# Kernel optimization log

Measured on AMD Instinct MI355X. Metric: run time of the kernel, lower is better.

The kernel has to match this reference:

```python
import jax, jax.numpy as jnp
import numpy as np

N_EMBD = 1024
HEAD_SIZE = 128


def setup_inputs() -> dict:
    key = jax.random.key(0)
    k_x, k_w, k_cov, k_b = jax.random.split(key, 4)
    x = jax.random.normal(k_x, (16384, 2, N_EMBD), dtype=jnp.float32)
    # values_proj: nn.Linear(n_embd, head_size, bias=False) -> weight [head_size, n_embd]
    W = jax.random.normal(k_w, (HEAD_SIZE, N_EMBD), dtype=jnp.float32) * (N_EMBD ** -0.5)
    cov = jax.random.normal(k_cov, (HEAD_SIZE, HEAD_SIZE), dtype=jnp.float32) * (HEAD_SIZE ** -0.5)
    bias = jax.random.normal(k_b, (HEAD_SIZE,), dtype=jnp.float32)
    return {"x": x, "W": W, "cov": cov, "bias": bias}


def reference(x, W, cov, bias):
    # x: [B, 2, E]; W: [H, E]; cov: [H, H]; bias: [H]
    values = jnp.einsum('be,he->bh', x[:, 0, :], W)  # [B, H]
    mask = jnp.einsum('be,he->bh', x[:, 1, :], W)    # [B, H]
    # diag_embed(mask) @ cov == mask[:, :, None] * cov  -> [B, H, H]
    coeffs = jax.nn.softmax(mask[:, :, None] * cov[None, :, :], axis=-1)
    # values.unsqueeze(1) @ coeffs + bias, then [:, 0, :]
    out = jnp.einsum('bh,bhk->bk', values, coeffs) + bias
    return out
```

## Files before the change

kernel.cpp:

```cpp
#include <hip/hip_runtime.h>
#include <hip/hip_bf16.h>

#define LOG2E 1.4426950408889634f

typedef __attribute__((ext_vector_type(8))) short frag_ab;
typedef __attribute__((ext_vector_type(4))) float frag_cd;

__device__ inline short f2bf(float f) {
    union { float f; unsigned u; } v; v.f = f;
    unsigned r = v.u + 0x7fffu + ((v.u >> 16) & 1u);
    return (short)(r >> 16);
}

__global__ __launch_bounds__(256) void prep_kernel(const float* __restrict__ W,
                                                   const float* __restrict__ cov,
                                                   short* __restrict__ wbf,
                                                   float* __restrict__ rmm) {
    if (blockIdx.x < 64) {
        int g = blockIdx.x * 256 + threadIdx.x;
        int h = g >> 7;
        int k0 = (g & 127) << 3;
        const float* src = W + h * 1024 + k0;
        float4 w0 = *(const float4*)src;
        float4 w1 = *(const float4*)(src + 4);
        frag_ab af;
        af[0] = f2bf(w0.x); af[1] = f2bf(w0.y); af[2] = f2bf(w0.z); af[3] = f2bf(w0.w);
        af[4] = f2bf(w1.x); af[5] = f2bf(w1.y); af[6] = f2bf(w1.z); af[7] = f2bf(w1.w);
        int c = k0 >> 6, s = (k0 >> 5) & 1, kg = (k0 >> 3) & 3;
        int nt = h >> 4, m = h & 15, lane = kg * 16 + m;
        int dst = (((c * 8 + nt) * 2 + s) * 64 + lane) * 8;
        *(frag_ab*)(wbf + dst) = af;
    } else {
        int h = blockIdx.x - 64;
        int lane = threadIdx.x;
        if (lane < 64) {
            float c1 = cov[h * 128 + lane];
            float c2 = cov[h * 128 + 64 + lane];
            float mx = fmaxf(c1, c2), mn = fminf(c1, c2);
            for (int o = 1; o < 64; o <<= 1) {
                mx = fmaxf(mx, __shfl_xor(mx, o, 64));
                mn = fminf(mn, __shfl_xor(mn, o, 64));
            }
            if (lane == 0) { rmm[h] = LOG2E * mx; rmm[128 + h] = LOG2E * mn; }
        }
    }
}

__global__ __launch_bounds__(256) void proj_kernel(const float* __restrict__ x,
                                                   const short* __restrict__ wbf,
                                                   float* __restrict__ vm) {
    const int tid = threadIdx.x;
    const int lane = tid & 63;
    const int wave = tid >> 6;
    const int m = lane & 15, kg = lane >> 4;
    const long rowbase = ((long)blockIdx.x * 4 + wave) * 16;
    const float* xrow = x + (rowbase + m) * 1024 + kg * 8;
    const char* wb = (const char*)wbf + lane * 16;

    frag_cd acc[8];
#pragma unroll
    for (int nt = 0; nt < 8; ++nt) acc[nt] = (frag_cd){0.f, 0.f, 0.f, 0.f};

    float4 a0 = *(const float4*)(xrow);
    float4 a1 = *(const float4*)(xrow + 4);
    float4 a2 = *(const float4*)(xrow + 32);
    float4 a3 = *(const float4*)(xrow + 36);

    for (int c = 0; c < 16; ++c) {
        frag_ab bfr[16];
        const char* bc = wb + c * 16384;
#pragma unroll
        for (int f = 0; f < 16; ++f)
            bfr[f] = *(const frag_ab*)(bc + f * 1024);

        float4 n0, n1, n2, n3;
        if (c < 15) {
            const float* xn = xrow + (c + 1) * 64;
            n0 = *(const float4*)(xn);
            n1 = *(const float4*)(xn + 4);
            n2 = *(const float4*)(xn + 32);
            n3 = *(const float4*)(xn + 36);
        }

        frag_ab af0, af1;
        af0[0] = f2bf(a0.x); af0[1] = f2bf(a0.y); af0[2] = f2bf(a0.z); af0[3] = f2bf(a0.w);
        af0[4] = f2bf(a1.x); af0[5] = f2bf(a1.y); af0[6] = f2bf(a1.z); af0[7] = f2bf(a1.w);
        af1[0] = f2bf(a2.x); af1[1] = f2bf(a2.y); af1[2] = f2bf(a2.z); af1[3] = f2bf(a2.w);
        af1[4] = f2bf(a3.x); af1[5] = f2bf(a3.y); af1[6] = f2bf(a3.z); af1[7] = f2bf(a3.w);

#pragma unroll
        for (int nt = 0; nt < 8; ++nt) {
            acc[nt] = __builtin_amdgcn_mfma_f32_16x16x32_bf16(af0, bfr[nt * 2 + 0], acc[nt], 0, 0, 0);
            acc[nt] = __builtin_amdgcn_mfma_f32_16x16x32_bf16(af1, bfr[nt * 2 + 1], acc[nt], 0, 0, 0);
        }
        if (c < 15) { a0 = n0; a1 = n1; a2 = n2; a3 = n3; }
    }

#pragma unroll
    for (int nt = 0; nt < 8; ++nt) {
#pragma unroll
        for (int r = 0; r < 4; ++r) {
            long row = rowbase + kg * 4 + r;
            vm[row * 128 + nt * 16 + m] = acc[nt][r];
        }
    }
}

__global__ __launch_bounds__(512, 4) void combine_kernel(const float* __restrict__ vm,
                                                         const float* __restrict__ cov,
                                                         const float* __restrict__ bias,
                                                         const float* __restrict__ rmm,
                                                         float* __restrict__ out, int B) {
    __shared__ float mask_s[128], m2_s[128], v_s[128];
    __shared__ float obuf[32][132];
    const int t = threadIdx.x;
    const int i = t >> 4;
    const int j = t & 15;

    float covreg[4][8];
#pragma unroll
    for (int hh = 0; hh < 4; ++hh) {
        const float* cr = cov + (long)(i * 4 + hh) * 128 + j * 8;
        float4 c0 = *(const float4*)cr;
        float4 c1 = *(const float4*)(cr + 4);
        covreg[hh][0] = LOG2E * c0.x; covreg[hh][1] = LOG2E * c0.y;
        covreg[hh][2] = LOG2E * c0.z; covreg[hh][3] = LOG2E * c0.w;
        covreg[hh][4] = LOG2E * c1.x; covreg[hh][5] = LOG2E * c1.y;
        covreg[hh][6] = LOG2E * c1.z; covreg[hh][7] = LOG2E * c1.w;
    }
    float rmax_own = 0.f, rmin_own = 0.f, bias_own = 0.f;
    if (t < 128) {
        rmax_own = rmm[t];
        rmin_own = rmm[128 + t];
        bias_own = bias[t];
    }

    for (int b = blockIdx.x; b < B; b += gridDim.x) {
        if (t < 128) {
            float val = vm[(long)(2 * b) * 128 + t];
            float mk  = vm[(long)(2 * b + 1) * 128 + t];
            v_s[t] = val;
            mask_s[t] = mk;
            m2_s[t] = mk * (mk >= 0.f ? rmax_own : rmin_own);
        }
        __syncthreads();

        float op[8] = {0.f, 0.f, 0.f, 0.f, 0.f, 0.f, 0.f, 0.f};
#pragma unroll
        for (int hh = 0; hh < 4; ++hh) {
            float mh = mask_s[i * 4 + hh];
            float mm = m2_s[i * 4 + hh];
            float p[8];
            float lsum = 0.f;
#pragma unroll
            for (int kk = 0; kk < 8; ++kk) {
                float e = __builtin_amdgcn_exp2f(fmaf(mh, covreg[hh][kk], -mm));
                p[kk] = e;
                lsum += e;
            }
            lsum += __shfl_xor(lsum, 1, 16);
            lsum += __shfl_xor(lsum, 2, 16);
            lsum += __shfl_xor(lsum, 4, 16);
            lsum += __shfl_xor(lsum, 8, 16);
            float w = v_s[i * 4 + hh] * __builtin_amdgcn_rcpf(lsum);
#pragma unroll
            for (int kk = 0; kk < 8; ++kk) op[kk] = fmaf(w, p[kk], op[kk]);
        }
        *(float4*)&obuf[i][j * 8]     = make_float4(op[0], op[1], op[2], op[3]);
        *(float4*)&obuf[i][j * 8 + 4] = make_float4(op[4], op[5], op[6], op[7]);
        __syncthreads();

        if (t < 128) {
            float o = 0.f;
#pragma unroll
            for (int ii = 0; ii < 32; ++ii) o += obuf[ii][t];
            out[(long)b * 128 + t] = o + bias_own;
        }
        __syncthreads();
    }
}

extern "C" void kernel_launch(void* const* d_in, const int* in_sizes, int n_in,
                              void* d_out, int out_size, void* d_ws, size_t ws_size,
                              hipStream_t stream) {
    const float* x    = (const float*)d_in[0];
    const float* W    = (const float*)d_in[1];
    const float* cov  = (const float*)d_in[2];
    const float* bias = (const float*)d_in[3];
    float* out = (float*)d_out;

    const int B = in_sizes[0] / (2 * 1024);

    float* vm  = (float*)d_ws;
    short* wbf = (short*)(vm + (size_t)2 * B * 128);
    float* rmm = (float*)(wbf + 128 * 1024);

    prep_kernel<<<192, 256, 0, stream>>>(W, cov, wbf, rmm);

    const int rows = 2 * B;
    const int blocks = rows / 64;
    proj_kernel<<<blocks, 256, 0, stream>>>(x, wbf, vm);

    combine_kernel<<<2048, 512, 0, stream>>>(vm, cov, bias, rmm, out, B);
}
```

Measured before the change: 296.1 us.

## Restructure softmax combine to one wave per batch with fp16 cov in LDS

Rewrites the combine kernel so each wave handles one batch row independently. The pre-scaled cov matrix is stored as fp16 in shared memory with a rotation to avoid bank conflicts, which removes the per-batch block barriers and the shared-memory reduction buffer. It also drops the softmax max subtraction, assuming the exponents stay bounded, and deepens the x prefetch pipeline in the projection kernel to three chunks. The trade-offs are lower cov precision and possible overflow for large mask values.

```diff
diff --git a/kernel.cpp b/kernel.cpp
--- a/kernel.cpp
+++ b/kernel.cpp
@@ -15,7 +15,7 @@
 __global__ __launch_bounds__(256) void prep_kernel(const float* __restrict__ W,
                                                    const float* __restrict__ cov,
                                                    short* __restrict__ wbf,
-                                                   float* __restrict__ rmm) {
+                                                   unsigned short* __restrict__ covh) {
     if (blockIdx.x < 64) {
         int g = blockIdx.x * 256 + threadIdx.x;
         int h = g >> 7;
@@ -31,24 +31,24 @@
         int dst = (((c * 8 + nt) * 2 + s) * 64 + lane) * 8;
         *(frag_ab*)(wbf + dst) = af;
     } else {
-        int h = blockIdx.x - 64;
-        int lane = threadIdx.x;
-        if (lane < 64) {
-            float c1 = cov[h * 128 + lane];
-            float c2 = cov[h * 128 + 64 + lane];
-            float mx = fmaxf(c1, c2), mn = fminf(c1, c2);
-            for (int o = 1; o < 64; o <<= 1) {
-                mx = fmaxf(mx, __shfl_xor(mx, o, 64));
-                mn = fminf(mn, __shfl_xor(mn, o, 64));
-            }
-            if (lane == 0) { rmm[h] = LOG2E * mx; rmm[128 + h] = LOG2E * mn; }
-        }
-    }
-}
-
-__global__ __launch_bounds__(256) void proj_kernel(const float* __restrict__ x,
-                                                   const short* __restrict__ wbf,
-                                                   float* __restrict__ vm) {
+        int t = threadIdx.x;
+        int h = t >> 1;
+        int k0 = (t & 1) * 64;
+        const float* cr = cov + h * 128 + k0;
+        int rot = 16 * (h >> 5);
+        for (int k = 0; k < 64; ++k) {
+            float c = cr[k] * LOG2E;
+            union { _Float16 hf; unsigned short us; } cu;
+            cu.hf = (_Float16)c;
+            int p = (k0 + k + rot) & 127;
+            covh[h * 128 + p] = cu.us;
+        }
+    }
+}
+
+__global__ __launch_bounds__(256, 2) void proj_kernel(const float* __restrict__ x,
+                                                      const short* __restrict__ wbf,
+                                                      float* __restrict__ vm) {
     const int tid = threadIdx.x;
     const int lane = tid & 63;
     const int wave = tid >> 6;
@@ -61,11 +61,17 @@
 #pragma unroll
     for (int nt = 0; nt < 8; ++nt) acc[nt] = (frag_cd){0.f, 0.f, 0.f, 0.f};
 
-    float4 a0 = *(const float4*)(xrow);
-    float4 a1 = *(const float4*)(xrow + 4);
-    float4 a2 = *(const float4*)(xrow + 32);
-    float4 a3 = *(const float4*)(xrow + 36);
-
+    float4 aq[4][4];
+#pragma unroll
+    for (int pc = 0; pc < 3; ++pc) {
+        const float* xn = xrow + pc * 64;
+        aq[pc][0] = *(const float4*)(xn);
+        aq[pc][1] = *(const float4*)(xn + 4);
+        aq[pc][2] = *(const float4*)(xn + 32);
+        aq[pc][3] = *(const float4*)(xn + 36);
+    }
+
+#pragma unroll
     for (int c = 0; c < 16; ++c) {
         frag_ab bfr[16];
         const char* bc = wb + c * 16384;
@@ -73,15 +79,16 @@
         for (int f = 0; f < 16; ++f)
             bfr[f] = *(const frag_ab*)(bc + f * 1024);
 
-        float4 n0, n1, n2, n3;
-        if (c < 15) {
-            const float* xn = xrow + (c + 1) * 64;
-            n0 = *(const float4*)(xn);
-            n1 = *(const float4*)(xn + 4);
-            n2 = *(const float4*)(xn + 32);
-            n3 = *(const float4*)(xn + 36);
-        }
-
+        if (c + 3 < 16) {
+            const float* xn = xrow + (c + 3) * 64;
+            aq[(c + 3) & 3][0] = *(const float4*)(xn);
+            aq[(c + 3) & 3][1] = *(const float4*)(xn + 4);
+            aq[(c + 3) & 3][2] = *(const float4*)(xn + 32);
+            aq[(c + 3) & 3][3] = *(const float4*)(xn + 36);
+        }
+
+        float4 a0 = aq[c & 3][0], a1 = aq[c & 3][1];
+        float4 a2 = aq[c & 3][2], a3 = aq[c & 3][3];
         frag_ab af0, af1;
         af0[0] = f2bf(a0.x); af0[1] = f2bf(a0.y); af0[2] = f2bf(a0.z); af0[3] = f2bf(a0.w);
         af0[4] = f2bf(a1.x); af0[5] = f2bf(a1.y); af0[6] = f2bf(a1.z); af0[7] = f2bf(a1.w);
@@ -93,7 +100,6 @@
             acc[nt] = __builtin_amdgcn_mfma_f32_16x16x32_bf16(af0, bfr[nt * 2 + 0], acc[nt], 0, 0, 0);
             acc[nt] = __builtin_amdgcn_mfma_f32_16x16x32_bf16(af1, bfr[nt * 2 + 1], acc[nt], 0, 0, 0);
         }
-        if (c < 15) { a0 = n0; a1 = n1; a2 = n2; a3 = n3; }
     }
 
 #pragma unroll
@@ -106,77 +112,92 @@
     }
 }
 
-__global__ __launch_bounds__(512, 4) void combine_kernel(const float* __restrict__ vm,
-                                                         const float* __restrict__ cov,
+__global__ __launch_bounds__(256, 4) void combine_kernel(const float* __restrict__ vm,
+                                                         const unsigned short* __restrict__ covh,
                                                          const float* __restrict__ bias,
-                                                         const float* __restrict__ rmm,
                                                          float* __restrict__ out, int B) {
-    __shared__ float mask_s[128], m2_s[128], v_s[128];
-    __shared__ float obuf[32][132];
+    __shared__ __align__(16) unsigned short cov_s[128 * 128];
     const int t = threadIdx.x;
-    const int i = t >> 4;
-    const int j = t & 15;
-
-    float covreg[4][8];
-#pragma unroll
-    for (int hh = 0; hh < 4; ++hh) {
-        const float* cr = cov + (long)(i * 4 + hh) * 128 + j * 8;
-        float4 c0 = *(const float4*)cr;
-        float4 c1 = *(const float4*)(cr + 4);
-        covreg[hh][0] = LOG2E * c0.x; covreg[hh][1] = LOG2E * c0.y;
-        covreg[hh][2] = LOG2E * c0.z; covreg[hh][3] = LOG2E * c0.w;
-        covreg[hh][4] = LOG2E * c1.x; covreg[hh][5] = LOG2E * c1.y;
-        covreg[hh][6] = LOG2E * c1.z; covreg[hh][7] = LOG2E * c1.w;
-    }
-    float rmax_own = 0.f, rmin_own = 0.f, bias_own = 0.f;
-    if (t < 128) {
-        rmax_own = rmm[t];
-        rmin_own = rmm[128 + t];
-        bias_own = bias[t];
-    }
-
-    for (int b = blockIdx.x; b < B; b += gridDim.x) {
-        if (t < 128) {
-            float val = vm[(long)(2 * b) * 128 + t];
-            float mk  = vm[(long)(2 * b + 1) * 128 + t];
-            v_s[t] = val;
-            mask_s[t] = mk;
-            m2_s[t] = mk * (mk >= 0.f ? rmax_own : rmin_own);
-        }
-        __syncthreads();
+
+    {
+        const float4* cg = (const float4*)covh;
+        float4* cl = (float4*)cov_s;
+#pragma unroll
+        for (int q = 0; q < 8; ++q) cl[q * 256 + t] = cg[q * 256 + t];
+    }
+    __syncthreads();
+
+    const int lane = t & 63;
+    const int wavei = t >> 6;
+    const int i = lane >> 4;
+    const int j = lane & 15;
+
+    float biasr[8];
+#pragma unroll
+    for (int s = 0; s < 4; ++s) {
+        float2 bp = *(const float2*)(bias + 2 * j + 32 * s);
+        biasr[2 * s] = bp.x; biasr[2 * s + 1] = bp.y;
+    }
+    int colb[4];
+#pragma unroll
+    for (int s = 0; s < 4; ++s) colb[s] = ((2 * j + 32 * s + 16 * i) & 127) * 2;
+
+    const char* covb = (const char*)cov_s;
+    const int gw = blockIdx.x * 4 + wavei;
+    const int nw = gridDim.x * 4;
+
+    for (int b = gw; b < B; b += nw) {
+        const float* vrow = vm + (long)(2 * b) * 128 + 32 * i;
+        const float* mrow = vrow + 128;
+        float vv[32], mk[32];
+#pragma unroll
+        for (int q = 0; q < 8; ++q) {
+            float4 v4 = *(const float4*)(vrow + 4 * q);
+            vv[4 * q] = v4.x; vv[4 * q + 1] = v4.y; vv[4 * q + 2] = v4.z; vv[4 * q + 3] = v4.w;
+            float4 m4 = *(const float4*)(mrow + 4 * q);
+            mk[4 * q] = m4.x; mk[4 * q + 1] = m4.y; mk[4 * q + 2] = m4.z; mk[4 * q + 3] = m4.w;
+        }
 
         float op[8] = {0.f, 0.f, 0.f, 0.f, 0.f, 0.f, 0.f, 0.f};
 #pragma unroll
-        for (int hh = 0; hh < 4; ++hh) {
-            float mh = mask_s[i * 4 + hh];
-            float mm = m2_s[i * 4 + hh];
+        for (int tt = 0; tt < 32; ++tt) {
+            float mval = mk[tt];
+            int rb = (32 * i + tt) * 256;
             float p[8];
-            float lsum = 0.f;
-#pragma unroll
-            for (int kk = 0; kk < 8; ++kk) {
-                float e = __builtin_amdgcn_exp2f(fmaf(mh, covreg[hh][kk], -mm));
-                p[kk] = e;
-                lsum += e;
+            float ls = 0.f;
+#pragma unroll
+            for (int s = 0; s < 4; ++s) {
+                unsigned cc = *(const unsigned*)(covb + rb + colb[s]);
+                union { unsigned u; _Float16 h[2]; } cu; cu.u = cc;
+                float c0 = (float)cu.h[0], c1 = (float)cu.h[1];
+                float p0 = __builtin_amdgcn_exp2f(mval * c0);
+                float p1 = __builtin_amdgcn_exp2f(mval * c1);
+                p[2 * s] = p0; p[2 * s + 1] = p1;
+                ls += p0 + p1;
             }
-            lsum += __shfl_xor(lsum, 1, 16);
-            lsum += __shfl_xor(lsum, 2, 16);
-            lsum += __shfl_xor(lsum, 4, 16);
-            lsum += __shfl_xor(lsum, 8, 16);
-            float w = v_s[i * 4 + hh] * __builtin_amdgcn_rcpf(lsum);
-#pragma unroll
-            for (int kk = 0; kk < 8; ++kk) op[kk] = fmaf(w, p[kk], op[kk]);
-        }
-        *(float4*)&obuf[i][j * 8]     = make_float4(op[0], op[1], op[2], op[3]);
-        *(float4*)&obuf[i][j * 8 + 4] = make_float4(op[4], op[5], op[6], op[7]);
-        __syncthreads();
-
-        if (t < 128) {
-            float o = 0.f;
-#pragma unroll
-            for (int ii = 0; ii < 32; ++ii) o += obuf[ii][t];
-            out[(long)b * 128 + t] = o + bias_own;
-        }
-        __syncthreads();
+            ls += __shfl_xor(ls, 1, 16);
+            ls += __shfl_xor(ls, 2, 16);
+            ls += __shfl_xor(ls, 4, 16);
+            ls += __shfl_xor(ls, 8, 16);
+            float w = vv[tt] * __builtin_amdgcn_rcpf(ls);
+#pragma unroll
+            for (int u = 0; u < 8; ++u) op[u] = fmaf(w, p[u], op[u]);
+        }
+#pragma unroll
+        for (int u = 0; u < 8; ++u) {
+            op[u] += __shfl_xor(op[u], 16, 64);
+            op[u] += __shfl_xor(op[u], 32, 64);
+        }
+        if (lane < 16) {
+            float* ob = out + (long)b * 128;
+#pragma unroll
+            for (int s = 0; s < 4; ++s) {
+                float2 o2;
+                o2.x = op[2 * s] + biasr[2 * s];
+                o2.y = op[2 * s + 1] + biasr[2 * s + 1];
+                *(float2*)(ob + 2 * j + 32 * s) = o2;
+            }
+        }
     }
 }
 
@@ -193,13 +214,12 @@
 
     float* vm  = (float*)d_ws;
     short* wbf = (short*)(vm + (size_t)2 * B * 128);
-    float* rmm = (float*)(wbf + 128 * 1024);
-
-    prep_kernel<<<192, 256, 0, stream>>>(W, cov, wbf, rmm);
-
-    const int rows = 2 * B;
-    const int blocks = rows / 64;
+    unsigned short* covh = (unsigned short*)(wbf + 128 * 1024);
+
+    prep_kernel<<<65, 256, 0, stream>>>(W, cov, wbf, covh);
+
+    const int blocks = (2 * B) / 64;
     proj_kernel<<<blocks, 256, 0, stream>>>(x, wbf, vm);
 
-    combine_kernel<<<2048, 512, 0, stream>>>(vm, cov, bias, rmm, out, B);
-}
+    combine_kernel<<<1024, 256, 0, stream>>>(vm, covh, bias, out, B);
+}
```

After: 522.9 us. 1.77x slower.
